# Kernel tuning notes

Hardware: AMD Instinct MI355X
Metric: run time of the kernel (lower is better)

The kernel has to match this reference:

```python
import jax, jax.numpy as jnp
import numpy as np

N_NODES = 100000
N_EDGES = 2400000


def setup_inputs() -> dict:
    key = jax.random.key(0)
    ks = jax.random.split(key, 6)
    x = jax.random.normal(ks[0], (N_NODES, 2), dtype=jnp.float32)
    edge_index = jax.random.randint(ks[1], (2, N_EDGES), 0, N_NODES, dtype=jnp.int64)
    # GCNConv weights (glorot-ish scale) and zero biases
    W1 = jax.random.normal(ks[2], (2, 32), dtype=jnp.float32) * (1.0 / np.sqrt(2.0))
    b1 = jnp.zeros((32,), dtype=jnp.float32)
    W2 = jax.random.normal(ks[3], (32, 32), dtype=jnp.float32) * (1.0 / np.sqrt(32.0))
    b2 = jnp.zeros((32,), dtype=jnp.float32)
    W3 = jax.random.normal(ks[4], (32, 1), dtype=jnp.float32) * (1.0 / np.sqrt(32.0))
    b3 = jnp.zeros((1,), dtype=jnp.float32)
    return {"x": x, "edge_index": edge_index, "W1": W1, "b1": b1,
            "W2": W2, "b2": b2, "W3": W3, "b3": b3}


def reference(x, edge_index, W1, b1, W2, b2, W3, b3):
    N = x.shape[0]
    self_loops = jnp.arange(N, dtype=edge_index.dtype)
    src = jnp.concatenate([edge_index[0], self_loops])  # message sources
    dst = jnp.concatenate([edge_index[1], self_loops])  # aggregation targets
    # Symmetric GCN normalization: deg computed at target nodes (PyG gcn_norm)
    deg = jax.ops.segment_sum(jnp.ones_like(dst, dtype=x.dtype), dst, num_segments=N)
    dinv = jnp.where(deg > 0, jax.lax.rsqrt(deg), 0.0)
    norm = (dinv[src] * dinv[dst])[:, None]  # [E+N, 1]

    def gcn_layer(h, W, b):
        h = h @ W                                  # [N, out]
        msg = norm * h[src]                        # gather + scale
        agg = jax.ops.segment_sum(msg, dst, num_segments=N)  # scatter-add
        return agg + b

    h = jax.nn.relu(gcn_layer(x, W1, b1))
    h = jax.nn.relu(gcn_layer(h, W2, b2))
    out = gcn_layer(h, W3, b3)
    return out.reshape(-1)
```

## Files before the change

### kernel.cpp

```cpp
#include <hip/hip_runtime.h>

#define NN 100000
#define NE 2400000
#define NB 391
#define CAP 6912
#define EPB 4096
#define NBLK2 ((NE + EPB - 1) / EPB)

__device__ __forceinline__ int wexscan(int v, int lane) {
    int x = v;
#pragma unroll
    for (int off = 1; off < 64; off <<= 1) {
        int t = __shfl_up(x, off, 64);
        x += (lane >= off) ? t : 0;
    }
    return x - v;
}

__global__ __launch_bounds__(512) void k_hist(const int* __restrict__ ei,
        int* __restrict__ bh) {
    __shared__ int hist[NB];
    int tid = threadIdx.x;
    for (int i = tid; i < NB; i += 512) hist[i] = 0;
    __syncthreads();
    int base_e = blockIdx.x * EPB + tid * 8;
    if (base_e + 8 <= NE) {
        int4 da = *(const int4*)(ei + NE + base_e);
        int4 db = *(const int4*)(ei + NE + base_e + 4);
        atomicAdd(&hist[da.x >> 8], 1); atomicAdd(&hist[da.y >> 8], 1);
        atomicAdd(&hist[da.z >> 8], 1); atomicAdd(&hist[da.w >> 8], 1);
        atomicAdd(&hist[db.x >> 8], 1); atomicAdd(&hist[db.y >> 8], 1);
        atomicAdd(&hist[db.z >> 8], 1); atomicAdd(&hist[db.w >> 8], 1);
    }
    __syncthreads();
    for (int i = tid; i < NB; i += 512) bh[blockIdx.x * NB + i] = hist[i];
}

__global__ __launch_bounds__(256) void k_offscan(int* __restrict__ bh,
        int* __restrict__ tot) {
    __shared__ int wsum[4];
    int b = blockIdx.x, tid = threadIdx.x;
    int lane = tid & 63, wid = tid >> 6;
    int carry = 0;
#pragma unroll
    for (int r = 0; r < 3; ++r) {
        int blk = r * 256 + tid;
        int v = (blk < NBLK2) ? bh[blk * NB + b] : 0;
        int ex = wexscan(v, lane);
        if (lane == 63) wsum[wid] = ex + v;
        __syncthreads();
        int woff = 0, rt = 0;
#pragma unroll
        for (int i = 0; i < 4; ++i) {
            woff += (i < wid) ? wsum[i] : 0;
            rt += wsum[i];
        }
        if (blk < NBLK2) bh[blk * NB + b] = b * CAP + carry + woff + ex;
        carry += rt;
        __syncthreads();
    }
    if (tid == 0) tot[b] = carry;
}

__global__ __launch_bounds__(512) void k_scatter2(const int* __restrict__ ei,
        const int* __restrict__ bh, int* __restrict__ binned) {
    __shared__ int hist[NB], lbase[NB], myb[NB];
    __shared__ int stage[EPB];
    __shared__ unsigned short stageb[EPB];
    __shared__ int wsum[8];
    int tid = threadIdx.x;
    for (int i = tid; i < NB; i += 512) {
        hist[i] = 0;
        myb[i] = bh[blockIdx.x * NB + i];
    }
    __syncthreads();
    int base_e = blockIdx.x * EPB + tid * 8;
    int pk[8], bn[8], rk[8];
    if (base_e + 8 <= NE) {
        const int4* s4 = (const int4*)(ei + base_e);
        const int4* d4 = (const int4*)(ei + NE + base_e);
        int4 sa = s4[0], sb = s4[1], da = d4[0], db = d4[1];
        int ss[8] = {sa.x, sa.y, sa.z, sa.w, sb.x, sb.y, sb.z, sb.w};
        int dd[8] = {da.x, da.y, da.z, da.w, db.x, db.y, db.z, db.w};
#pragma unroll
        for (int k = 0; k < 8; ++k) {
            bn[k] = dd[k] >> 8;
            pk[k] = ss[k] | ((dd[k] & 255) << 17);
            rk[k] = atomicAdd(&hist[bn[k]], 1);
        }
    } else {
#pragma unroll
        for (int k = 0; k < 8; ++k) bn[k] = -1;
    }
    __syncthreads();
    int lane = tid & 63, wid = tid >> 6;
    int v = (tid < NB) ? hist[tid] : 0;
    int ex = wexscan(v, lane);
    if (lane == 63) wsum[wid] = ex + v;
    __syncthreads();
    int woff = 0, tot = 0;
#pragma unroll
    for (int i = 0; i < 8; ++i) {
        int s = wsum[i];
        woff += (i < wid) ? s : 0;
        tot += s;
    }
    ex += woff;
    if (tid < NB) lbase[tid] = ex;
    __syncthreads();
#pragma unroll
    for (int k = 0; k < 8; ++k) {
        if (bn[k] >= 0) {
            int slot = lbase[bn[k]] + rk[k];
            stage[slot] = pk[k];
            stageb[slot] = (unsigned short)bn[k];
        }
    }
    __syncthreads();
    for (int j = tid; j < tot; j += 512) {
        int b = stageb[j];
        binned[myb[b] + (j - lbase[b])] = stage[j];
    }
}

__global__ __launch_bounds__(256) void k_csr_count(const int* __restrict__ binned,
        const int* __restrict__ tot, const float* __restrict__ x,
        int* __restrict__ rsp, float* __restrict__ dinv, float2* __restrict__ xs) {
    __shared__ int cnt[256];
    __shared__ int wsum[4];
    int tid = threadIdx.x, b = blockIdx.x;
    int base = b * CAP, n = tot[b];
    cnt[tid] = 0;
    __syncthreads();
    int n4 = n >> 2;
    const int4* b4 = (const int4*)(binned + base);
    for (int j = tid; j < n4; j += 256) {
        int4 w = b4[j];
        atomicAdd(&cnt[(w.x >> 17) & 255], 1);
        atomicAdd(&cnt[(w.y >> 17) & 255], 1);
        atomicAdd(&cnt[(w.z >> 17) & 255], 1);
        atomicAdd(&cnt[(w.w >> 17) & 255], 1);
    }
    for (int j = (n4 << 2) + tid; j < n; j += 256)
        atomicAdd(&cnt[(binned[base + j] >> 17) & 255], 1);
    __syncthreads();
    int deg = cnt[tid];
    int lane = tid & 63, wid = tid >> 6;
    int ex = wexscan(deg, lane);
    if (lane == 63) wsum[wid] = ex + deg;
    __syncthreads();
    int woff = 0;
#pragma unroll
    for (int i = 0; i < 4; ++i) woff += (i < wid) ? wsum[i] : 0;
    ex += woff;
    int node = (b << 8) + tid;
    if (node < NN) {
        rsp[node] = ((base + ex) << 8) | deg;
        float di = rsqrtf((float)(deg + 1));
        dinv[node] = di;
        float2 xv = ((const float2*)x)[node];
        xs[node] = make_float2(di * xv.x, di * xv.y);
    }
}

__global__ __launch_bounds__(256) void k_csr_place(const int* __restrict__ binned,
        const int* __restrict__ tot, const int* __restrict__ rsp,
        const float2* __restrict__ xs, const float* __restrict__ dinv,
        int* __restrict__ csr, float4* __restrict__ At) {
    __shared__ int cur2[256];
    int tid = threadIdx.x, b = blockIdx.x;
    int base = b * CAP, n = tot[b];
    int node = (b << 8) + tid;
    int rp = (node < NN) ? rsp[node] : 0;
    cur2[tid] = (node < NN) ? ((rp >> 8) - base) : 0;
    __syncthreads();
    int n4 = n >> 2;
    const int4* b4 = (const int4*)(binned + base);
    for (int j = tid; j < n4; j += 256) {
        int4 w = b4[j];
        int p0 = atomicAdd(&cur2[(w.x >> 17) & 255], 1); csr[base + p0] = w.x & 0x1FFFF;
        int p1 = atomicAdd(&cur2[(w.y >> 17) & 255], 1); csr[base + p1] = w.y & 0x1FFFF;
        int p2 = atomicAdd(&cur2[(w.z >> 17) & 255], 1); csr[base + p2] = w.z & 0x1FFFF;
        int p3 = atomicAdd(&cur2[(w.w >> 17) & 255], 1); csr[base + p3] = w.w & 0x1FFFF;
    }
    for (int j = (n4 << 2) + tid; j < n; j += 256) {
        int w = binned[base + j];
        int p = atomicAdd(&cur2[(w >> 17) & 255], 1);
        csr[base + p] = w & 0x1FFFF;
    }
    __syncthreads();
    if (node < NN) {
        int beg = rp >> 8, deg = rp & 255;
        float ax = 0.f, ay = 0.f;
        int e = beg, end = beg + deg;
        for (; e + 4 <= end; e += 4) {
            int s0 = csr[e], s1 = csr[e + 1], s2 = csr[e + 2], s3 = csr[e + 3];
            float2 v0 = xs[s0], v1 = xs[s1], v2 = xs[s2], v3 = xs[s3];
            ax += (v0.x + v1.x) + (v2.x + v3.x);
            ay += (v0.y + v1.y) + (v2.y + v3.y);
        }
        for (; e < end; ++e) { float2 vv = xs[csr[e]]; ax += vv.x; ay += vv.y; }
        float di = dinv[node];
        float2 xn = xs[node];
        At[node] = make_float4(di * (ax + xn.x), di * (ay + xn.y), di, 0.f);
    }
}

__global__ __launch_bounds__(256) void k_gather_fly(const float4* __restrict__ At,
        const int* __restrict__ rsp, const int* __restrict__ csr,
        const float* __restrict__ W1, const float* __restrict__ b1,
        const float* __restrict__ W2, const float* __restrict__ b2,
        const float* __restrict__ W3, float* __restrict__ h3) {
    __shared__ float WsT[32 * 36];
    __shared__ float accS[256];
    __shared__ float4 stage[8][32];
    int tid = threadIdx.x;
    for (int j = tid; j < 1024; j += 256) {
        int k = j >> 5, fo = j & 31;
        WsT[fo * 36 + k] = W2[j];
    }
    int g = tid >> 5, f = tid & 31;
    int node = blockIdx.x * 8 + g;
    float w0f = W1[f], w1f = W1[32 + f], bf = b1[f];
    float4 an = At[node];
    int r = rsp[node];
    float di = an.z;
    float vs = fmaf(an.y, w1f, fmaf(an.x, w0f, bf));
    float acc0 = di * fmaxf(vs, 0.f), acc1 = 0.f;
    int beg = r >> 8, deg = r & 255;
    float4* st = &stage[g][0];
    for (int b0 = 0; b0 < deg; b0 += 32) {
        float4 a = make_float4(0.f, 0.f, 0.f, 0.f);
        if (b0 + f < deg) a = At[csr[beg + b0 + f]];
        st[f] = a;
        __asm__ __volatile__("" ::: "memory");
#pragma unroll
        for (int j = 0; j < 32; j += 2) {
            float4 e0 = st[j], e1 = st[j + 1];
            float v0 = fmaf(e0.y, w1f, fmaf(e0.x, w0f, bf));
            acc0 = fmaf(e0.z, fmaxf(v0, 0.f), acc0);
            float v1 = fmaf(e1.y, w1f, fmaf(e1.x, w0f, bf));
            acc1 = fmaf(e1.z, fmaxf(v1, 0.f), acc1);
        }
        __asm__ __volatile__("" ::: "memory");
    }
    accS[tid] = di * (acc0 + acc1);
    __syncthreads();
    int n0 = tid & 224;
    float sum = b2[f];
    const float* wrow = &WsT[f * 36];
#pragma unroll
    for (int k = 0; k < 32; k += 4) {
        float4 a4 = *(const float4*)&accS[n0 + k];
        float4 w4 = *(const float4*)&wrow[k];
        sum = fmaf(a4.x, w4.x, sum);
        sum = fmaf(a4.y, w4.y, sum);
        sum = fmaf(a4.z, w4.z, sum);
        sum = fmaf(a4.w, w4.w, sum);
    }
    float h2 = fmaxf(sum, 0.f);
    float v = di * h2 * W3[f];
#pragma unroll
    for (int off = 16; off > 0; off >>= 1) v += __shfl_down(v, off, 32);
    if (f == 0) h3[node] = v;
}

__global__ __launch_bounds__(256) void k_gather_out(const float* __restrict__ hs,
        const int* __restrict__ rsp, const int* __restrict__ csr,
        const float* __restrict__ dinv, const float* __restrict__ bias,
        float* __restrict__ out) {
    int node = blockIdx.x * 256 + threadIdx.x;
    if (node >= NN) return;
    int r = rsp[node];
    int beg = r >> 8, end = beg + (r & 255);
    float acc = hs[node];
    int e = beg;
    for (; e + 4 <= end; e += 4) {
        int s0 = csr[e], s1 = csr[e + 1], s2 = csr[e + 2], s3 = csr[e + 3];
        acc += (hs[s0] + hs[s1]) + (hs[s2] + hs[s3]);
    }
    for (; e < end; ++e) acc += hs[csr[e]];
    out[node] = dinv[node] * acc + bias[0];
}

extern "C" void kernel_launch(void* const* d_in, const int* in_sizes, int n_in,
                              void* d_out, int out_size, void* d_ws, size_t ws_size,
                              hipStream_t stream) {
    const float* x  = (const float*)d_in[0];
    const int*   ei = (const int*)d_in[1];
    const float* W1 = (const float*)d_in[2];
    const float* b1 = (const float*)d_in[3];
    const float* W2 = (const float*)d_in[4];
    const float* b2 = (const float*)d_in[5];
    const float* W3 = (const float*)d_in[6];
    const float* b3 = (const float*)d_in[7];
    float* out = (float*)d_out;

    char* w = (char*)d_ws;
    float4* At    = (float4*)w; w += NN * 16;
    float2* xs    = (float2*)w; w += NN * 8;
    int*   bh     = (int*)w;    w += NBLK2 * NB * 4;
    int*   tot    = (int*)w;    w += NB * 4;
    int*   rsp    = (int*)w;    w += NN * 4;
    float* dinv   = (float*)w;  w += NN * 4;
    int*   binned = (int*)w;    w += NB * CAP * 4;
    int*   csr    = (int*)w;    w += NB * CAP * 4;
    float* h3     = (float*)w;  w += NN * 4;

    const int G_N = (NN + 255) / 256;
    const int G_G = NN / 8;

    k_hist<<<NBLK2, 512, 0, stream>>>(ei, bh);
    k_offscan<<<NB, 256, 0, stream>>>(bh, tot);
    k_scatter2<<<NBLK2, 512, 0, stream>>>(ei, bh, binned);
    k_csr_count<<<NB, 256, 0, stream>>>(binned, tot, x, rsp, dinv, xs);
    k_csr_place<<<NB, 256, 0, stream>>>(binned, tot, rsp, xs, dinv, csr, At);
    k_gather_fly<<<G_G, 256, 0, stream>>>(At, rsp, csr, W1, b1, W2, b2, W3, h3);
    k_gather_out<<<G_N, 256, 0, stream>>>(h3, rsp, csr, dinv, b3, out);
}
```

Baseline: 185.3 us.

## Remap layer-2 gather to 8 threads per node with 4 features each

Rewrites the fused layer-1/layer-2 aggregation kernel so each node is handled by 8 threads that each compute 4 of the 32 hidden features, with 32 nodes per block instead of 8. Each thread loads neighbor At entries directly, four at a time with masked tails, rather than staging them through shared memory per 32-thread group. W2 columns are kept in registers for the 32x32 matmul. This cuts the redundant per-feature recomputation and shared-memory staging, and increases memory-level parallelism. The cost is more registers per thread and redundant At loads across the 8 threads of a node. The csr buffer is padded so the 4-wide over-read stays in bounds.

```diff
diff --git a/kernel.cpp b/kernel.cpp
--- a/kernel.cpp
+++ b/kernel.cpp
@@ -206,63 +206,95 @@
     }
 }
 
-__global__ __launch_bounds__(256) void k_gather_fly(const float4* __restrict__ At,
+__global__ __launch_bounds__(256) void k_agg(const float4* __restrict__ At,
         const int* __restrict__ rsp, const int* __restrict__ csr,
         const float* __restrict__ W1, const float* __restrict__ b1,
         const float* __restrict__ W2, const float* __restrict__ b2,
         const float* __restrict__ W3, float* __restrict__ h3) {
-    __shared__ float WsT[32 * 36];
-    __shared__ float accS[256];
-    __shared__ float4 stage[8][32];
+    __shared__ float accS[32 * 36];
+    __shared__ float diS[32];
     int tid = threadIdx.x;
-    for (int j = tid; j < 1024; j += 256) {
-        int k = j >> 5, fo = j & 31;
-        WsT[fo * 36 + k] = W2[j];
-    }
-    int g = tid >> 5, f = tid & 31;
-    int node = blockIdx.x * 8 + g;
-    float w0f = W1[f], w1f = W1[32 + f], bf = b1[f];
+    int o = tid & 7, nl = tid >> 3;
+    int node = blockIdx.x * 32 + nl;
+    int f = tid & 31;
+
+    float4 w0 = *(const float4*)&W1[4 * o];
+    float4 w1 = *(const float4*)&W1[32 + 4 * o];
+    float4 bb = *(const float4*)&b1[4 * o];
+
+    int r = rsp[node];
+    int beg = r >> 8, deg = r & 255;
     float4 an = At[node];
-    int r = rsp[node];
     float di = an.z;
-    float vs = fmaf(an.y, w1f, fmaf(an.x, w0f, bf));
-    float acc0 = di * fmaxf(vs, 0.f), acc1 = 0.f;
-    int beg = r >> 8, deg = r & 255;
-    float4* st = &stage[g][0];
-    for (int b0 = 0; b0 < deg; b0 += 32) {
-        float4 a = make_float4(0.f, 0.f, 0.f, 0.f);
-        if (b0 + f < deg) a = At[csr[beg + b0 + f]];
-        st[f] = a;
-        __asm__ __volatile__("" ::: "memory");
-#pragma unroll
-        for (int j = 0; j < 32; j += 2) {
-            float4 e0 = st[j], e1 = st[j + 1];
-            float v0 = fmaf(e0.y, w1f, fmaf(e0.x, w0f, bf));
-            acc0 = fmaf(e0.z, fmaxf(v0, 0.f), acc0);
-            float v1 = fmaf(e1.y, w1f, fmaf(e1.x, w0f, bf));
-            acc1 = fmaf(e1.z, fmaxf(v1, 0.f), acc1);
-        }
-        __asm__ __volatile__("" ::: "memory");
-    }
-    accS[tid] = di * (acc0 + acc1);
-    __syncthreads();
-    int n0 = tid & 224;
-    float sum = b2[f];
-    const float* wrow = &WsT[f * 36];
-#pragma unroll
-    for (int k = 0; k < 32; k += 4) {
-        float4 a4 = *(const float4*)&accS[n0 + k];
-        float4 w4 = *(const float4*)&wrow[k];
-        sum = fmaf(a4.x, w4.x, sum);
-        sum = fmaf(a4.y, w4.y, sum);
-        sum = fmaf(a4.z, w4.z, sum);
-        sum = fmaf(a4.w, w4.w, sum);
-    }
-    float h2 = fmaxf(sum, 0.f);
-    float v = di * h2 * W3[f];
-#pragma unroll
-    for (int off = 16; off > 0; off >>= 1) v += __shfl_down(v, off, 32);
-    if (f == 0) h3[node] = v;
+
+    float4 acc;
+    {
+        float v0 = fmaf(an.y, w1.x, fmaf(an.x, w0.x, bb.x));
+        float v1 = fmaf(an.y, w1.y, fmaf(an.x, w0.y, bb.y));
+        float v2 = fmaf(an.y, w1.z, fmaf(an.x, w0.z, bb.z));
+        float v3 = fmaf(an.y, w1.w, fmaf(an.x, w0.w, bb.w));
+        acc.x = di * fmaxf(v0, 0.f);
+        acc.y = di * fmaxf(v1, 0.f);
+        acc.z = di * fmaxf(v2, 0.f);
+        acc.w = di * fmaxf(v3, 0.f);
+    }
+
+    auto acc1 = [&](const float4& aa, float zz) {
+        float v0 = fmaf(aa.y, w1.x, fmaf(aa.x, w0.x, bb.x));
+        float v1 = fmaf(aa.y, w1.y, fmaf(aa.x, w0.y, bb.y));
+        float v2 = fmaf(aa.y, w1.z, fmaf(aa.x, w0.z, bb.z));
+        float v3 = fmaf(aa.y, w1.w, fmaf(aa.x, w0.w, bb.w));
+        acc.x = fmaf(zz, fmaxf(v0, 0.f), acc.x);
+        acc.y = fmaf(zz, fmaxf(v1, 0.f), acc.y);
+        acc.z = fmaf(zz, fmaxf(v2, 0.f), acc.z);
+        acc.w = fmaf(zz, fmaxf(v3, 0.f), acc.w);
+    };
+
+    for (int j = 0; j < deg; j += 4) {
+        int e = beg + j;
+        int t0 = csr[e];
+        int t1 = csr[e + 1], t2 = csr[e + 2], t3 = csr[e + 3];
+        int s1 = (j + 1 < deg) ? t1 : 0;
+        int s2 = (j + 2 < deg) ? t2 : 0;
+        int s3 = (j + 3 < deg) ? t3 : 0;
+        float m1 = (j + 1 < deg) ? 1.f : 0.f;
+        float m2 = (j + 2 < deg) ? 1.f : 0.f;
+        float m3 = (j + 3 < deg) ? 1.f : 0.f;
+        float4 a0 = At[t0], a1 = At[s1], a2 = At[s2], a3 = At[s3];
+        float z0 = a0.z, z1 = m1 * a1.z, z2 = m2 * a2.z, z3 = m3 * a3.z;
+        acc1(a0, z0); acc1(a1, z1); acc1(a2, z2); acc1(a3, z3);
+    }
+
+    float w2r[32];
+#pragma unroll
+    for (int k = 0; k < 32; ++k) w2r[k] = W2[k * 32 + f];
+
+    acc.x *= di; acc.y *= di; acc.z *= di; acc.w *= di;
+    *(float4*)&accS[nl * 36 + 4 * o] = acc;
+    if (o == 0) diS[nl] = di;
+    __syncthreads();
+
+    float bf = b2[f], w3f = W3[f];
+    int g = tid >> 5;
+#pragma unroll
+    for (int rr = 0; rr < 4; ++rr) {
+        int n = g + 8 * rr;
+        const float* arow = &accS[n * 36];
+        float sum = bf;
+#pragma unroll
+        for (int k = 0; k < 32; k += 4) {
+            float4 a4 = *(const float4*)&arow[k];
+            sum = fmaf(a4.x, w2r[k], sum);
+            sum = fmaf(a4.y, w2r[k + 1], sum);
+            sum = fmaf(a4.z, w2r[k + 2], sum);
+            sum = fmaf(a4.w, w2r[k + 3], sum);
+        }
+        float h2 = fmaxf(sum, 0.f);
+        float v = h2 * w3f;
+#pragma unroll
+        for (int off = 16; off > 0; off >>= 1) v += __shfl_down(v, off, 32);
+        if (f == 0) h3[blockIdx.x * 32 + n] = diS[n] * v;
+    }
 }
 
 __global__ __launch_bounds__(256) void k_gather_out(const float* __restrict__ hs,
@@ -304,17 +336,17 @@
     int*   rsp    = (int*)w;    w += NN * 4;
     float* dinv   = (float*)w;  w += NN * 4;
     int*   binned = (int*)w;    w += NB * CAP * 4;
-    int*   csr    = (int*)w;    w += NB * CAP * 4;
+    int*   csr    = (int*)w;    w += (NB * CAP + 16) * 4;
     float* h3     = (float*)w;  w += NN * 4;
 
     const int G_N = (NN + 255) / 256;
-    const int G_G = NN / 8;
+    const int G_A = NN / 32;
 
     k_hist<<<NBLK2, 512, 0, stream>>>(ei, bh);
     k_offscan<<<NB, 256, 0, stream>>>(bh, tot);
     k_scatter2<<<NBLK2, 512, 0, stream>>>(ei, bh, binned);
     k_csr_count<<<NB, 256, 0, stream>>>(binned, tot, x, rsp, dinv, xs);
     k_csr_place<<<NB, 256, 0, stream>>>(binned, tot, rsp, xs, dinv, csr, At);
-    k_gather_fly<<<G_G, 256, 0, stream>>>(At, rsp, csr, W1, b1, W2, b2, W3, h3);
+    k_agg<<<G_A, 256, 0, stream>>>(At, rsp, csr, W1, b1, W2, b2, W3, h3);
     k_gather_out<<<G_N, 256, 0, stream>>>(h3, rsp, csr, dinv, b3, out);
 }
```

Result: faster. 171.2 us (-7.7%).
